# Kernel tuning notes

Measured on AMD Instinct MI355X. Metric: run time of the kernel, lower is better.

The kernel has to match this reference:

```python
import jax, jax.numpy as jnp
import numpy as np

GROUP_SIZE = 64  # quantization group size along in_features
RANK = 16
ALPHA = 1.0


def setup_inputs() -> dict:
    key = jax.random.key(0)
    ks = jax.random.split(key, 7)
    B, S, D_in, D_out = 4, 2048, 4096, 4096
    n_groups = D_in // GROUP_SIZE
    x = jax.random.normal(ks[0], (B, S, D_in), dtype=jnp.float32)
    qweight = jax.random.randint(ks[1], (D_out, D_in), 0, 16, dtype=jnp.int32)
    scales = jax.random.uniform(ks[2], (D_out, n_groups), dtype=jnp.float32) * 0.02
    zeros = jax.random.uniform(ks[3], (D_out, n_groups), dtype=jnp.float32) * 16.0
    lora_A = jax.random.normal(ks[4], (RANK, D_in), dtype=jnp.float32) / np.sqrt(D_in)
    lora_B = jax.random.normal(ks[5], (D_out, RANK), dtype=jnp.float32) * 0.01
    bias = jax.random.normal(ks[6], (D_out,), dtype=jnp.float32) * 0.02
    return {"x": x, "qweight": qweight, "scales": scales, "zeros": zeros,
            "lora_A": lora_A, "lora_B": lora_B, "bias": bias}


def _dequant(qweight, scales, zeros):
    # qweight: [O, I] int codes in [0,16); scales/zeros: [O, G] with G = I // GROUP_SIZE
    O, I = qweight.shape
    G = I // GROUP_SIZE
    q = qweight.astype(scales.dtype).reshape(O, G, GROUP_SIZE)
    w = (q - zeros[:, :, None]) * scales[:, :, None]
    return w.reshape(O, I)


def reference(x, qweight, scales, zeros, lora_A, lora_B, bias):
    # Base 4-bit dequantized matmul: y = x @ W^T
    W = _dequant(qweight, scales, zeros)            # [O, I]
    y = jnp.einsum('bsi,oi->bso', x, W)             # [B, S, O]
    # LoRA low-rank update: (alpha / rank) * (x @ A^T) @ B^T
    scaling = ALPHA / RANK
    lora = jnp.einsum('bsr,or->bso', jnp.einsum('bsi,ri->bsr', x, lora_A), lora_B)
    return y + scaling * lora + bias
```

## Files before the change

kernel.cpp:

```cpp
#include <hip/hip_runtime.h>
#include <stdint.h>
#include <stddef.h>

#define GM 8192
#define GN 4096
#define GK 4096
#define NGRP 64

typedef __bf16 bf16;
typedef __attribute__((ext_vector_type(8))) __bf16 bf16x8;
typedef __attribute__((ext_vector_type(4))) __bf16 bf16x4;
typedef __attribute__((ext_vector_type(4))) float floatx4;
typedef __attribute__((ext_vector_type(4))) int   intx4;
typedef __attribute__((ext_vector_type(8))) unsigned short ushortx8;
typedef __attribute__((ext_vector_type(4))) unsigned short ushortx4;

__device__ inline unsigned short f2bf(float f) {
  unsigned int u = __builtin_bit_cast(unsigned int, f);
  u += 0x7FFFu + ((u >> 16) & 1u);
  return (unsigned short)(u >> 16);
}

__device__ inline bf16x8 pack8(floatx4 a, floatx4 b) {
  ushortx8 u;
  u[0]=f2bf(a[0]); u[1]=f2bf(a[1]); u[2]=f2bf(a[2]); u[3]=f2bf(a[3]);
  u[4]=f2bf(b[0]); u[5]=f2bf(b[1]); u[6]=f2bf(b[2]); u[7]=f2bf(b[3]);
  return __builtin_bit_cast(bf16x8, u);
}

__device__ inline bf16x4 pack4(floatx4 a) {
  ushortx4 u;
  u[0]=f2bf(a[0]); u[1]=f2bf(a[1]); u[2]=f2bf(a[2]); u[3]=f2bf(a[3]);
  return __builtin_bit_cast(bf16x4, u);
}

__device__ inline void gll16(const void* g, void* l) {
  __builtin_amdgcn_global_load_lds(
      (const __attribute__((address_space(1))) void*)g,
      (__attribute__((address_space(3))) void*)l, 16, 0, 0);
}

__global__ void qlora_prep_x(const float* __restrict__ x, bf16* __restrict__ xbf) {
  size_t i = ((size_t)blockIdx.x * 256 + threadIdx.x) * 8;
  floatx4 a = *(const floatx4*)(x + i);
  floatx4 b = *(const floatx4*)(x + i + 4);
  *(bf16x8*)(xbf + i) = pack8(a, b);
}

__global__ void qlora_prep_w(const int* __restrict__ qw, const float* __restrict__ scales,
                             const float* __restrict__ zeros, const float* __restrict__ lA,
                             const float* __restrict__ lB, bf16* __restrict__ wbf) {
  __shared__ __align__(16) float Al[16 * 512];
  __shared__ __align__(16) float Bl[64 * 16];
  const int n0  = blockIdx.x * 64;
  const int kc0 = blockIdx.y * 512;
  const int tid = threadIdx.x;
  for (int t = 0; t < 8; ++t) {
    int idx = tid + t * 256;
    int r = idx >> 7, c = idx & 127;
    *(floatx4*)&Al[r * 512 + c * 4] = *(const floatx4*)&lA[(size_t)r * GK + kc0 + c * 4];
  }
  {
    int r = tid >> 2, c = tid & 3;
    *(floatx4*)&Bl[r * 16 + c * 4] = *(const floatx4*)&lB[(size_t)(n0 + r) * 16 + c * 4];
  }
  __syncthreads();

  const int klane = tid & 63;
  const int rowgrp = tid >> 6;
  for (int it = 0; it < 16; ++it) {
    int nl = rowgrp * 16 + it;
    int n  = n0 + nl;
    float Bv[16];
    #pragma unroll
    for (int r = 0; r < 16; ++r) Bv[r] = Bl[nl * 16 + r];
    #pragma unroll
    for (int half = 0; half < 2; ++half) {
      int k = klane * 4 + half * 256;
      floatx4 lacc = {0.f, 0.f, 0.f, 0.f};
      #pragma unroll
      for (int r = 0; r < 16; ++r) {
        floatx4 av = *(const floatx4*)&Al[r * 512 + k];
        lacc += av * Bv[r];
      }
      intx4 qv = *(const intx4*)&qw[(size_t)n * GK + kc0 + k];
      int g = (kc0 + k) >> 6;
      float s = scales[n * NGRP + g];
      float z = zeros[n * NGRP + g];
      floatx4 w;
      w[0] = ((float)qv[0] - z) * s + 0.0625f * lacc[0];
      w[1] = ((float)qv[1] - z) * s + 0.0625f * lacc[1];
      w[2] = ((float)qv[2] - z) * s + 0.0625f * lacc[2];
      w[3] = ((float)qv[3] - z) * s + 0.0625f * lacc[3];
      *(bf16x4*)&wbf[(size_t)n * GK + kc0 + k] = pack4(w);
    }
  }
}

template <bool APRE, bool WPRE>
__global__ void qlora_gemm(const bf16* __restrict__ Abf, const bf16* __restrict__ Wbf,
                           const float* __restrict__ x, const int* __restrict__ qw,
                           const float* __restrict__ scales, const float* __restrict__ zeros,
                           const float* __restrict__ bias, float* __restrict__ out) {
  __shared__ __align__(16) bf16 As[128 * 64];
  __shared__ __align__(16) bf16 Bs[128 * 64];
  const int tid  = threadIdx.x;
  const int wave = tid >> 6;
  const int lane = tid & 63;
  const int m0 = blockIdx.x * 128;
  const int n0 = blockIdx.y * 128;
  const int wm = (wave >> 1) * 64;
  const int wn = (wave & 1) * 64;

  floatx4 acc[4][4] = {};

  for (int k0 = 0; k0 < GK; k0 += 64) {
    if constexpr (APRE) {
      #pragma unroll
      for (int i = 0; i < 4; ++i) {
        int rb = (wave * 4 + i) * 8;
        const char* g = (const char*)(Abf + (size_t)(m0 + rb + (lane >> 3)) * GK + k0)
                        + (lane & 7) * 16;
        gll16(g, (char*)As + rb * 128);
      }
    } else {
      int row = tid >> 1, kh = (tid & 1) * 32;
      const float* gx = x + (size_t)(m0 + row) * GK + k0 + kh;
      #pragma unroll
      for (int j = 0; j < 4; ++j) {
        floatx4 a = *(const floatx4*)(gx + j * 8);
        floatx4 b = *(const floatx4*)(gx + j * 8 + 4);
        *(bf16x8*)&As[row * 64 + kh + j * 8] = pack8(a, b);
      }
    }
    if constexpr (WPRE) {
      #pragma unroll
      for (int i = 0; i < 4; ++i) {
        int rb = (wave * 4 + i) * 8;
        const char* g = (const char*)(Wbf + (size_t)(n0 + rb + (lane >> 3)) * GK + k0)
                        + (lane & 7) * 16;
        gll16(g, (char*)Bs + rb * 128);
      }
    } else {
      int row = tid >> 1, kh = (tid & 1) * 32;
      int n = n0 + row;
      int g = k0 >> 6;
      float s = scales[n * NGRP + g];
      float z = zeros[n * NGRP + g];
      const int* gq = qw + (size_t)n * GK + k0 + kh;
      #pragma unroll
      for (int j = 0; j < 4; ++j) {
        intx4 q0 = *(const intx4*)(gq + j * 8);
        intx4 q1 = *(const intx4*)(gq + j * 8 + 4);
        floatx4 a, b;
        a[0]=((float)q0[0]-z)*s; a[1]=((float)q0[1]-z)*s; a[2]=((float)q0[2]-z)*s; a[3]=((float)q0[3]-z)*s;
        b[0]=((float)q1[0]-z)*s; b[1]=((float)q1[1]-z)*s; b[2]=((float)q1[2]-z)*s; b[3]=((float)q1[3]-z)*s;
        *(bf16x8*)&Bs[row * 64 + kh + j * 8] = pack8(a, b);
      }
    }
    __syncthreads();

    #pragma unroll
    for (int kk = 0; kk < 64; kk += 32) {
      bf16x8 af[4], bfr[4];
      #pragma unroll
      for (int i = 0; i < 4; ++i)
        af[i] = *(const bf16x8*)&As[(wm + i * 16 + (lane & 15)) * 64 + kk + (lane >> 4) * 8];
      #pragma unroll
      for (int i = 0; i < 4; ++i)
        bfr[i] = *(const bf16x8*)&Bs[(wn + i * 16 + (lane & 15)) * 64 + kk + (lane >> 4) * 8];
      #pragma unroll
      for (int mi = 0; mi < 4; ++mi)
        #pragma unroll
        for (int ni = 0; ni < 4; ++ni)
          acc[mi][ni] = __builtin_amdgcn_mfma_f32_16x16x32_bf16(af[mi], bfr[ni], acc[mi][ni], 0, 0, 0);
    }
    __syncthreads();
  }

  const int quad = lane >> 4;
  const int col  = lane & 15;
  #pragma unroll
  for (int ni = 0; ni < 4; ++ni) {
    int gn = n0 + wn + ni * 16 + col;
    float bv = bias[gn];
    #pragma unroll
    for (int mi = 0; mi < 4; ++mi) {
      int gm = m0 + wm + mi * 16 + quad * 4;
      #pragma unroll
      for (int r = 0; r < 4; ++r)
        out[(size_t)(gm + r) * GN + gn] = acc[mi][ni][r] + bv;
    }
  }
}

extern "C" void kernel_launch(void* const* d_in, const int* in_sizes, int n_in,
                              void* d_out, int out_size, void* d_ws, size_t ws_size,
                              hipStream_t stream) {
  (void)in_sizes; (void)n_in; (void)out_size;
  const float* x      = (const float*)d_in[0];
  const int*   qw     = (const int*)d_in[1];
  const float* scales = (const float*)d_in[2];
  const float* zeros  = (const float*)d_in[3];
  const float* lA     = (const float*)d_in[4];
  const float* lB     = (const float*)d_in[5];
  const float* bias   = (const float*)d_in[6];
  float* out = (float*)d_out;

  const size_t xbf_bytes = (size_t)GM * GK * sizeof(bf16);
  const size_t wbf_bytes = (size_t)GN * GK * sizeof(bf16);
  char* ws = (char*)d_ws;

  bf16* xbf = nullptr;
  bf16* wbf = nullptr;
  bool apre = false, wpre = false;
  if (ws_size >= xbf_bytes + wbf_bytes) {
    apre = wpre = true;
    xbf = (bf16*)ws;
    wbf = (bf16*)(ws + xbf_bytes);
  } else if (ws_size >= wbf_bytes) {
    wpre = true;
    wbf = (bf16*)ws;
  }

  if (apre)
    qlora_prep_x<<<dim3((GM * GK) / (256 * 8)), 256, 0, stream>>>(x, xbf);
  if (wpre)
    qlora_prep_w<<<dim3(GN / 64, GK / 512), 256, 0, stream>>>(qw, scales, zeros, lA, lB, wbf);

  dim3 grid(GM / 128, GN / 128);
  if (apre && wpre)
    qlora_gemm<true, true><<<grid, 256, 0, stream>>>(xbf, wbf, x, qw, scales, zeros, bias, out);
  else if (wpre)
    qlora_gemm<false, true><<<grid, 256, 0, stream>>>(xbf, wbf, x, qw, scales, zeros, bias, out);
  else
    qlora_gemm<false, false><<<grid, 256, 0, stream>>>(xbf, wbf, x, qw, scales, zeros, bias, out);
}
```

Baseline: 614.2 us.

## Swizzle LDS tile layout, fuse prep kernels, and remap blocks across XCDs

Stores the bf16 copies of x and W in global memory with an XOR swizzle of 8-element chunks keyed on row, so the direct global-to-LDS loads land already swizzled. The MFMA fragment reads from LDS apply the matching XOR to avoid bank conflicts. The two prep kernels are merged into one launch, and GEMM block indices are remapped so each XCD handles a contiguous band of N tiles for better L2 reuse. The fallback path that only pre-converted W is removed, and the swizzle must stay consistent across prep, the non-prep path and the reads.

```diff
diff --git a/kernel.cpp b/kernel.cpp
--- a/kernel.cpp
+++ b/kernel.cpp
@@ -20,41 +20,44 @@
   u += 0x7FFFu + ((u >> 16) & 1u);
   return (unsigned short)(u >> 16);
 }
-
 __device__ inline bf16x8 pack8(floatx4 a, floatx4 b) {
   ushortx8 u;
   u[0]=f2bf(a[0]); u[1]=f2bf(a[1]); u[2]=f2bf(a[2]); u[3]=f2bf(a[3]);
   u[4]=f2bf(b[0]); u[5]=f2bf(b[1]); u[6]=f2bf(b[2]); u[7]=f2bf(b[3]);
   return __builtin_bit_cast(bf16x8, u);
 }
-
 __device__ inline bf16x4 pack4(floatx4 a) {
   ushortx4 u;
   u[0]=f2bf(a[0]); u[1]=f2bf(a[1]); u[2]=f2bf(a[2]); u[3]=f2bf(a[3]);
   return __builtin_bit_cast(bf16x4, u);
 }
-
 __device__ inline void gll16(const void* g, void* l) {
   __builtin_amdgcn_global_load_lds(
       (const __attribute__((address_space(1))) void*)g,
       (__attribute__((address_space(3))) void*)l, 16, 0, 0);
 }
 
-__global__ void qlora_prep_x(const float* __restrict__ x, bf16* __restrict__ xbf) {
-  size_t i = ((size_t)blockIdx.x * 256 + threadIdx.x) * 8;
-  floatx4 a = *(const floatx4*)(x + i);
-  floatx4 b = *(const floatx4*)(x + i + 4);
-  *(bf16x8*)(xbf + i) = pack8(a, b);
-}
-
-__global__ void qlora_prep_w(const int* __restrict__ qw, const float* __restrict__ scales,
-                             const float* __restrict__ zeros, const float* __restrict__ lA,
-                             const float* __restrict__ lB, bf16* __restrict__ wbf) {
+__global__ void qlora_prep(const float* __restrict__ x, bf16* __restrict__ xbf,
+                           const int* __restrict__ qw, const float* __restrict__ scales,
+                           const float* __restrict__ zeros, const float* __restrict__ lA,
+                           const float* __restrict__ lB, bf16* __restrict__ wbf) {
   __shared__ __align__(16) float Al[16 * 512];
   __shared__ __align__(16) float Bl[64 * 16];
-  const int n0  = blockIdx.x * 64;
-  const int kc0 = blockIdx.y * 512;
   const int tid = threadIdx.x;
+  if (blockIdx.x < 16384) {
+    int fc = blockIdx.x * 256 + tid;
+    int m  = fc >> 9;
+    int rc = fc & 511;
+    int p  = (rc & 7) ^ (m & 7);
+    const float* src = x + ((size_t)fc << 3);
+    floatx4 a = *(const floatx4*)src;
+    floatx4 b = *(const floatx4*)(src + 4);
+    *(bf16x8*)(xbf + (size_t)m * GK + ((rc >> 3) << 6) + (p << 3)) = pack8(a, b);
+    return;
+  }
+  const int wb  = blockIdx.x - 16384;
+  const int n0  = (wb & 63) * 64;
+  const int kc0 = (wb >> 6) * 512;
   for (int t = 0; t < 8; ++t) {
     int idx = tid + t * 256;
     int r = idx >> 7, c = idx & 127;
@@ -66,7 +69,7 @@
   }
   __syncthreads();
 
-  const int klane = tid & 63;
+  const int klane  = tid & 63;
   const int rowgrp = tid >> 6;
   for (int it = 0; it < 16; ++it) {
     int nl = rowgrp * 16 + it;
@@ -84,7 +87,8 @@
         lacc += av * Bv[r];
       }
       intx4 qv = *(const intx4*)&qw[(size_t)n * GK + kc0 + k];
-      int g = (kc0 + k) >> 6;
+      int kg = kc0 + k;
+      int g  = kg >> 6;
       float s = scales[n * NGRP + g];
       float z = zeros[n * NGRP + g];
       floatx4 w;
@@ -92,7 +96,9 @@
       w[1] = ((float)qv[1] - z) * s + 0.0625f * lacc[1];
       w[2] = ((float)qv[2] - z) * s + 0.0625f * lacc[2];
       w[3] = ((float)qv[3] - z) * s + 0.0625f * lacc[3];
-      *(bf16x4*)&wbf[(size_t)n * GK + kc0 + k] = pack4(w);
+      int kb = kg & ~63;
+      int p  = (((kg >> 3) & 7) ^ (n & 7)) << 3;
+      *(bf16x4*)&wbf[(size_t)n * GK + kb + p + (kg & 7)] = pack4(w);
     }
   }
 }
@@ -107,10 +113,14 @@
   const int tid  = threadIdx.x;
   const int wave = tid >> 6;
   const int lane = tid & 63;
-  const int m0 = blockIdx.x * 128;
-  const int n0 = blockIdx.y * 128;
+  const int flat = blockIdx.y * gridDim.x + blockIdx.x;
+  const int xcd  = flat & 7;
+  const int j    = flat >> 3;
+  const int m0   = (j >> 2) * 128;
+  const int n0   = (xcd * 4 + (j & 3)) * 128;
   const int wm = (wave >> 1) * 64;
   const int wn = (wave & 1) * 64;
+  const int rsw = lane & 7;
 
   floatx4 acc[4][4] = {};
 
@@ -127,10 +137,11 @@
       int row = tid >> 1, kh = (tid & 1) * 32;
       const float* gx = x + (size_t)(m0 + row) * GK + k0 + kh;
       #pragma unroll
-      for (int j = 0; j < 4; ++j) {
-        floatx4 a = *(const floatx4*)(gx + j * 8);
-        floatx4 b = *(const floatx4*)(gx + j * 8 + 4);
-        *(bf16x8*)&As[row * 64 + kh + j * 8] = pack8(a, b);
+      for (int jj = 0; jj < 4; ++jj) {
+        floatx4 a = *(const floatx4*)(gx + jj * 8);
+        floatx4 b = *(const floatx4*)(gx + jj * 8 + 4);
+        int p = (((kh >> 3) + jj) ^ (row & 7)) << 3;
+        *(bf16x8*)&As[row * 64 + p] = pack8(a, b);
       }
     }
     if constexpr (WPRE) {
@@ -149,26 +160,30 @@
       float z = zeros[n * NGRP + g];
       const int* gq = qw + (size_t)n * GK + k0 + kh;
       #pragma unroll
-      for (int j = 0; j < 4; ++j) {
-        intx4 q0 = *(const intx4*)(gq + j * 8);
-        intx4 q1 = *(const intx4*)(gq + j * 8 + 4);
+      for (int jj = 0; jj < 4; ++jj) {
+        intx4 q0 = *(const intx4*)(gq + jj * 8);
+        intx4 q1 = *(const intx4*)(gq + jj * 8 + 4);
         floatx4 a, b;
         a[0]=((float)q0[0]-z)*s; a[1]=((float)q0[1]-z)*s; a[2]=((float)q0[2]-z)*s; a[3]=((float)q0[3]-z)*s;
         b[0]=((float)q1[0]-z)*s; b[1]=((float)q1[1]-z)*s; b[2]=((float)q1[2]-z)*s; b[3]=((float)q1[3]-z)*s;
-        *(bf16x8*)&Bs[row * 64 + kh + j * 8] = pack8(a, b);
+        int p = (((kh >> 3) + jj) ^ (row & 7)) << 3;
+        *(bf16x8*)&Bs[row * 64 + p] = pack8(a, b);
       }
     }
     __syncthreads();
 
     #pragma unroll
     for (int kk = 0; kk < 64; kk += 32) {
+      const int cbase = kk >> 3;
       bf16x8 af[4], bfr[4];
       #pragma unroll
       for (int i = 0; i < 4; ++i)
-        af[i] = *(const bf16x8*)&As[(wm + i * 16 + (lane & 15)) * 64 + kk + (lane >> 4) * 8];
+        af[i] = *(const bf16x8*)&As[(wm + i * 16 + (lane & 15)) * 64
+                                    + (((cbase + (lane >> 4)) ^ rsw) << 3)];
       #pragma unroll
       for (int i = 0; i < 4; ++i)
-        bfr[i] = *(const bf16x8*)&Bs[(wn + i * 16 + (lane & 15)) * 64 + kk + (lane >> 4) * 8];
+        bfr[i] = *(const bf16x8*)&Bs[(wn + i * 16 + (lane & 15)) * 64
+                                     + (((cbase + (lane >> 4)) ^ rsw) << 3)];
       #pragma unroll
       for (int mi = 0; mi < 4; ++mi)
         #pragma unroll
@@ -211,28 +226,13 @@
   const size_t wbf_bytes = (size_t)GN * GK * sizeof(bf16);
   char* ws = (char*)d_ws;
 
-  bf16* xbf = nullptr;
-  bf16* wbf = nullptr;
-  bool apre = false, wpre = false;
+  dim3 grid(GM / 128, GN / 128);
   if (ws_size >= xbf_bytes + wbf_bytes) {
-    apre = wpre = true;
-    xbf = (bf16*)ws;
-    wbf = (bf16*)(ws + xbf_bytes);
-  } else if (ws_size >= wbf_bytes) {
-    wpre = true;
-    wbf = (bf16*)ws;
-  }
-
-  if (apre)
-    qlora_prep_x<<<dim3((GM * GK) / (256 * 8)), 256, 0, stream>>>(x, xbf);
-  if (wpre)
-    qlora_prep_w<<<dim3(GN / 64, GK / 512), 256, 0, stream>>>(qw, scales, zeros, lA, lB, wbf);
-
-  dim3 grid(GM / 128, GN / 128);
-  if (apre && wpre)
+    bf16* xbf = (bf16*)ws;
+    bf16* wbf = (bf16*)(ws + xbf_bytes);
+    qlora_prep<<<dim3(16384 + 512), 256, 0, stream>>>(x, xbf, qw, scales, zeros, lA, lB, wbf);
     qlora_gemm<true, true><<<grid, 256, 0, stream>>>(xbf, wbf, x, qw, scales, zeros, bias, out);
-  else if (wpre)
-    qlora_gemm<false, true><<<grid, 256, 0, stream>>>(xbf, wbf, x, qw, scales, zeros, bias, out);
-  else
-    qlora_gemm<false, false><<<grid, 256, 0, stream>>>(xbf, wbf, x, qw, scales, zeros, bias, out);
-}
+  } else {
+    qlora_gemm<false, false><<<grid, 256, 0, stream>>>(nullptr, nullptr, x, qw, scales, zeros, bias, out);
+  }
+}
```

Result: slower. 637.1 us (+3.7%).
